# Kernel tuning notes

Hardware: AMD Instinct MI355X
Metric: run time of the kernel (lower is better)

The kernel has to match this reference:

```python
import jax, jax.numpy as jnp
import numpy as np

EPS = 0.4          # attack step size (init eps)
TOP_K_FRAC = 0.5   # fraction of tokens kept by gradient magnitude
STD_MULT = 3.0     # outlier threshold in stds
COS_EPS = 1e-8     # torch cosine_similarity norm clamp

B, S, E, V = 32, 64, 512, 50257


def setup_inputs() -> dict:
    key = jax.random.key(0)
    k1, k2, k3 = jax.random.split(key, 3)
    utterance = jax.random.randint(k1, (B, S), 0, V)
    emb_table = jax.random.normal(k2, (V, E), dtype=jnp.float32)
    data_grad = jax.random.normal(k3, (B, S, E), dtype=jnp.float32) * 0.01
    return {"utterance": utterance, "emb_table": emb_table, "data_grad": data_grad}


def fgsm_attack(inputs, data_grad):
    # inputs, data_grad: [B, S, E]
    b, s, e = data_grad.shape
    abs_grad = jnp.abs(data_grad).sum(axis=-1)                # [B, S]
    k = int(TOP_K_FRAC * s)
    _, top_idx = jax.lax.top_k(abs_grad, k)                   # [B, k], descending
    tok_mask = jnp.zeros((b, s), dtype=bool).at[jnp.arange(b)[:, None], top_idx].set(True)
    mask = jnp.broadcast_to(tok_mask[:, :, None], data_grad.shape)  # [B, S, E]
    g = jnp.where(mask, data_grad, 0.0)
    n = b * k * e                                             # number of kept gradient entries
    mean = g.sum() / n
    var = (jnp.where(mask, data_grad - mean, 0.0) ** 2).sum() / (n - 1)  # unbiased (torch.std)
    std = jnp.sqrt(var)
    lb, ub = mean - std * STD_MULT, mean + std * STD_MULT
    outside = (data_grad < lb) | (data_grad > ub)
    g2 = jnp.where(mask & outside, data_grad, 0.0)
    return inputs + EPS * jnp.sign(g2)


def reference(utterance, emb_table, data_grad):
    # embedding lookup: in_data = embeddings(utterance)
    in_data = emb_table[utterance]                            # [B, S, E]
    perturbed = fgsm_attack(in_data, data_grad)               # [B, S, E]
    # batched cosine similarity of every perturbed token vs full vocab
    p_norm = jnp.maximum(jnp.linalg.norm(perturbed, axis=-1), COS_EPS)   # [B, S]
    t_norm = jnp.maximum(jnp.linalg.norm(emb_table, axis=-1), COS_EPS)   # [V]
    sim = jnp.einsum("bse,ve->bsv", perturbed, emb_table)
    sim = sim / (p_norm[:, :, None] * t_norm[None, None, :])  # [B, S, V]
    # nearest-neighbor token ids (deterministic first-of-ties, replaces random tie sampling)
    nn_idx = jnp.argmax(sim, axis=-1)                         # [B, S]
    return nn_idx, sim
```

## Files before the change

kernel.cpp:

```cpp
#include <hip/hip_runtime.h>

#define B_      32
#define S_      64
#define E_      512
#define V_      50257
#define NPAD_   50304
#define M_      2048
#define NMASK_  524288.0
#define EPS_    0.4f

typedef _Float16 half8 __attribute__((ext_vector_type(8)));
typedef float f32x4 __attribute__((ext_vector_type(4)));

__device__ __forceinline__ float wave_sum(float s) {
#pragma unroll
    for (int d = 32; d; d >>= 1) s += __shfl_xor(s, d);
    return s;
}

__global__ void k_absgrad(const float* __restrict__ grad, float* __restrict__ absg) {
    const int row = blockIdx.x * 4 + (threadIdx.x >> 6);
    const int ln  = threadIdx.x & 63;
    const float4* g = (const float4*)(grad + (size_t)row * E_) + ln * 2;
    float4 a = g[0], b = g[1];
    float s = fabsf(a.x) + fabsf(a.y) + fabsf(a.z) + fabsf(a.w)
            + fabsf(b.x) + fabsf(b.y) + fabsf(b.z) + fabsf(b.w);
    s = wave_sum(s);
    if (ln == 0) absg[row] = s;
}

__global__ void k_topk(const float* __restrict__ absg, int* __restrict__ mask) {
    __shared__ float sh[S_];
    const int b = blockIdx.x, s = threadIdx.x;
    const float v = absg[b * S_ + s];
    sh[s] = v;
    __syncthreads();
    int rank = 0;
#pragma unroll
    for (int t = 0; t < S_; ++t) {
        float o = sh[t];
        rank += (o > v) || (o == v && t < s);
    }
    mask[b * S_ + s] = (rank < 32);
}

__global__ void k_stats1(const float* __restrict__ grad, const int* __restrict__ mask,
                         float* __restrict__ part) {
    const int tid = threadIdx.x;
    float s1 = 0.f, s2 = 0.f;
    for (int i = blockIdx.x * 256 + tid; i < M_ * E_; i += 128 * 256) {
        if (mask[i >> 9]) {
            float x = grad[i];
            s1 += x; s2 += x * x;
        }
    }
    s1 = wave_sum(s1); s2 = wave_sum(s2);
    __shared__ float r1[4], r2[4];
    if ((tid & 63) == 0) { r1[tid >> 6] = s1; r2[tid >> 6] = s2; }
    __syncthreads();
    if (tid == 0) {
        part[2 * blockIdx.x]     = r1[0] + r1[1] + r1[2] + r1[3];
        part[2 * blockIdx.x + 1] = r2[0] + r2[1] + r2[2] + r2[3];
    }
}

__global__ void k_stats2(const float* __restrict__ part, float* __restrict__ stats) {
    if (threadIdx.x == 0) {
        double s1 = 0.0, s2 = 0.0;
        for (int i = 0; i < 128; ++i) { s1 += part[2 * i]; s2 += part[2 * i + 1]; }
        const double n = NMASK_;
        double mean = s1 / n;
        double var  = (s2 - s1 * s1 / n) / (n - 1.0);
        double sd   = sqrt(var);
        stats[0] = (float)(mean - 3.0 * sd);
        stats[1] = (float)(mean + 3.0 * sd);
    }
}

__global__ void k_pert(const float* __restrict__ grad, const float* __restrict__ emb,
                       const int* __restrict__ utt, const int* __restrict__ mask,
                       const float* __restrict__ stats,
                       _Float16* __restrict__ pf16, float* __restrict__ inv_p) {
    const int row = blockIdx.x * 4 + (threadIdx.x >> 6);
    const int ln  = threadIdx.x & 63;
    const int tok = utt[row];
    const int msk = mask[row];
    const float lb = stats[0], ub = stats[1];
    const float* gp = grad + (size_t)row * E_ + ln * 8;
    const float* ep = emb + (size_t)tok * E_ + ln * 8;
    float4 g0 = *(const float4*)gp, g1 = *(const float4*)(gp + 4);
    float4 e0 = *(const float4*)ep, e1 = *(const float4*)(ep + 4);
    float gx[8] = {g0.x, g0.y, g0.z, g0.w, g1.x, g1.y, g1.z, g1.w};
    float ex[8] = {e0.x, e0.y, e0.z, e0.w, e1.x, e1.y, e1.z, e1.w};
    half8 h;
    float ss = 0.f;
#pragma unroll
    for (int i = 0; i < 8; ++i) {
        float x = gx[i];
        float val = ex[i];
        if (msk && (x < lb || x > ub)) val += (x > 0.f) ? EPS_ : -EPS_;
        ss += val * val;
        h[i] = (_Float16)val;
    }
    *(half8*)(pf16 + (size_t)row * E_ + ln * 8) = h;
    ss = wave_sum(ss);
    if (ln == 0) inv_p[row] = 1.f / fmaxf(sqrtf(ss), 1e-8f);
}

__global__ void k_emb(const float* __restrict__ emb, _Float16* __restrict__ ef16,
                      float* __restrict__ inv_t) {
    const int row = blockIdx.x * 4 + (threadIdx.x >> 6);
    const int ln  = threadIdx.x & 63;
    half8 h;
    float ss = 0.f;
    if (row < V_) {
        const float* ep = emb + (size_t)row * E_ + ln * 8;
        float4 e0 = *(const float4*)ep, e1 = *(const float4*)(ep + 4);
        float ex[8] = {e0.x, e0.y, e0.z, e0.w, e1.x, e1.y, e1.z, e1.w};
#pragma unroll
        for (int i = 0; i < 8; ++i) { ss += ex[i] * ex[i]; h[i] = (_Float16)ex[i]; }
    } else {
#pragma unroll
        for (int i = 0; i < 8; ++i) h[i] = (_Float16)0.f;
    }
    *(half8*)(ef16 + (size_t)row * E_ + ln * 8) = h;
    ss = wave_sum(ss);
    if (ln == 0) inv_t[row] = (row < V_) ? 1.f / fmaxf(sqrtf(ss), 1e-8f) : 0.f;
}

__device__ __forceinline__ void glds16(const _Float16* g, void* l) {
    __builtin_amdgcn_global_load_lds(
        (const __attribute__((address_space(1))) void*)g,
        (__attribute__((address_space(3))) void*)l, 16, 0, 0);
}

__global__ __launch_bounds__(256) void k_gemm(
    const _Float16* __restrict__ A,
    const _Float16* __restrict__ Bm,
    const float* __restrict__ inv_p,
    const float* __restrict__ inv_t,
    float* __restrict__ simout,
    unsigned long long* __restrict__ keys) {
    __shared__ _Float16 As[128][32];
    __shared__ _Float16 Bs[128][32];
    const int tid = threadIdx.x;
    const int wv = tid >> 6, ln = tid & 63;
    const int m0 = blockIdx.y * 128, n0 = blockIdx.x * 128;
    const int wr = wv >> 1, wc = wv & 1;
    const int lr = ln & 15, lk = (ln >> 4) * 8;

    f32x4 acc[4][4];
#pragma unroll
    for (int i = 0; i < 4; ++i)
#pragma unroll
        for (int j = 0; j < 4; ++j) acc[i][j] = (f32x4){0.f, 0.f, 0.f, 0.f};

    const int srow = wv * 16 + (ln >> 2);
    const int scol = (ln & 3) * 8;
    const _Float16* gA = A  + (size_t)(m0 + srow) * E_ + scol;
    const _Float16* gB = Bm + (size_t)(n0 + srow) * E_ + scol;
    char* lA = (char*)&As[0][0] + wv * 1024;
    char* lB = (char*)&Bs[0][0] + wv * 1024;

    for (int k0 = 0; k0 < E_; k0 += 32) {
        glds16(gA + k0,            lA);
        glds16(gA + 64 * E_ + k0,  lA + 4096);
        glds16(gB + k0,            lB);
        glds16(gB + 64 * E_ + k0,  lB + 4096);
        __syncthreads();
        half8 af[4], bf[4];
#pragma unroll
        for (int f = 0; f < 4; ++f) {
            af[f] = *(const half8*)&As[wr * 64 + f * 16 + lr][lk];
            bf[f] = *(const half8*)&Bs[wc * 64 + f * 16 + lr][lk];
        }
#pragma unroll
        for (int i = 0; i < 4; ++i)
#pragma unroll
            for (int j = 0; j < 4; ++j)
                acc[i][j] = __builtin_amdgcn_mfma_f32_16x16x32_f16(af[i], bf[j], acc[i][j], 0, 0, 0);
        __syncthreads();
    }

    int vv[4];
    float itv[4];
#pragma unroll
    for (int fn = 0; fn < 4; ++fn) {
        vv[fn] = n0 + wc * 64 + fn * 16 + lr;
        itv[fn] = inv_t[vv[fn]];
    }
#pragma unroll
    for (int fm = 0; fm < 4; ++fm) {
#pragma unroll
        for (int j = 0; j < 4; ++j) {
            const int m = m0 + wr * 64 + fm * 16 + (ln >> 4) * 4 + j;
            const float ip = inv_p[m];
            float* orow = simout + (size_t)m * V_;
            unsigned long long best = 0ull;
#pragma unroll
            for (int fn = 0; fn < 4; ++fn) {
                const int v = vv[fn];
                if (v < V_) {
                    const float sv = acc[fm][fn][j] * ip * itv[fn];
                    orow[v] = sv;
                    unsigned u = __float_as_uint(sv);
                    u = (u & 0x80000000u) ? ~u : (u | 0x80000000u);
                    unsigned long long e = ((unsigned long long)u << 32) | (unsigned)(~v);
                    best = e > best ? e : best;
                }
            }
#pragma unroll
            for (int d = 1; d < 16; d <<= 1) {
                unsigned long long o = __shfl_xor(best, d);
                best = o > best ? o : best;
            }
            if (lr == 0) atomicMax(keys + m, best);
        }
    }
}

__global__ void k_idx(const unsigned long long* __restrict__ keys, float* __restrict__ out) {
    const int i = blockIdx.x * 256 + threadIdx.x;
    if (i < M_) {
        unsigned v = ~(unsigned)(keys[i] & 0xFFFFFFFFull);
        out[i] = (float)v;
    }
}

extern "C" void kernel_launch(void* const* d_in, const int* in_sizes, int n_in,
                              void* d_out, int out_size, void* d_ws, size_t ws_size,
                              hipStream_t stream) {
    const int*   utt  = (const int*)d_in[0];
    const float* emb  = (const float*)d_in[1];
    const float* grad = (const float*)d_in[2];

    char* ws = (char*)d_ws;
    _Float16* embF16  = (_Float16*)(ws);
    _Float16* pertF16 = (_Float16*)(ws + 51511296);
    float* inv_t = (float*)(ws + 53608448);
    float* inv_p = (float*)(ws + 53809664);
    float* absg  = (float*)(ws + 53817856);
    int*   mask  = (int*)  (ws + 53826048);
    float* part  = (float*)(ws + 53834240);
    float* stats = (float*)(ws + 53835264);
    unsigned long long* keys = (unsigned long long*)(ws + 53835520);

    float* outIdx = (float*)d_out;
    float* simout = (float*)d_out + M_;

    hipMemsetAsync(keys, 0, M_ * 8, stream);
    k_absgrad<<<M_ / 4, 256, 0, stream>>>(grad, absg);
    k_topk<<<B_, S_, 0, stream>>>(absg, mask);
    k_stats1<<<128, 256, 0, stream>>>(grad, mask, part);
    k_stats2<<<1, 64, 0, stream>>>(part, stats);
    k_pert<<<M_ / 4, 256, 0, stream>>>(grad, emb, utt, mask, stats, pertF16, inv_p);
    k_emb<<<NPAD_ / 4, 256, 0, stream>>>(emb, embF16, inv_t);
    k_gemm<<<dim3(NPAD_ / 128, M_ / 128), 256, 0, stream>>>(pertF16, embF16, inv_p, inv_t, simout, keys);
    k_idx<<<8, 256, 0, stream>>>(keys, outIdx);
}
```

Before: 963.9 us.

## Double-buffer GEMM LDS tiles, swizzle workgroups across XCDs, parallelize stats reduction

The GEMM main loop now uses two LDS buffers, so the global-to-LDS load for the next K slice is issued before the MFMAs on the current slice run. This halves the barriers per iteration and lets loads overlap with compute. The 2D grid becomes a 1D grid whose block ids are remapped, so consecutive workgroups on the same XCD share nearby M/N tiles and should get better L2 reuse. The single-thread stats reduction is also replaced by a wave-wide shuffle reduction in double precision. The cost is twice the LDS per block, which may lower occupancy.

```diff
diff --git a/kernel.cpp b/kernel.cpp
--- a/kernel.cpp
+++ b/kernel.cpp
@@ -8,6 +8,8 @@
 #define M_      2048
 #define NMASK_  524288.0
 #define EPS_    0.4f
+#define NWG_    6288
+#define CPX_    786
 
 typedef _Float16 half8 __attribute__((ext_vector_type(8)));
 typedef float f32x4 __attribute__((ext_vector_type(4)));
@@ -65,9 +67,19 @@
 }
 
 __global__ void k_stats2(const float* __restrict__ part, float* __restrict__ stats) {
-    if (threadIdx.x == 0) {
-        double s1 = 0.0, s2 = 0.0;
-        for (int i = 0; i < 128; ++i) { s1 += part[2 * i]; s2 += part[2 * i + 1]; }
+    const int ln = threadIdx.x & 63;
+    double s1 = 0.0, s2 = 0.0;
+    if (ln < 32) { s1 = part[2 * ln]; s2 = part[2 * ln + 1]; }
+    if (ln + 64 < 128) { }
+    s1 += (double)part[2 * (ln + 64)];
+    s2 += (double)part[2 * (ln + 64) + 1];
+    if (ln >= 32) { s1 += (double)part[2 * ln]; s2 += (double)part[2 * ln + 1]; }
+#pragma unroll
+    for (int d = 32; d; d >>= 1) {
+        s1 += __shfl_xor(s1, d);
+        s2 += __shfl_xor(s2, d);
+    }
+    if (ln == 0) {
         const double n = NMASK_;
         double mean = s1 / n;
         double var  = (s2 - s1 * s1 / n) / (n - 1.0);
@@ -141,11 +153,16 @@
     const float* __restrict__ inv_t,
     float* __restrict__ simout,
     unsigned long long* __restrict__ keys) {
-    __shared__ _Float16 As[128][32];
-    __shared__ _Float16 Bs[128][32];
+    __shared__ _Float16 As[2][128][32];
+    __shared__ _Float16 Bs[2][128][32];
     const int tid = threadIdx.x;
     const int wv = tid >> 6, ln = tid & 63;
-    const int m0 = blockIdx.y * 128, n0 = blockIdx.x * 128;
+
+    const int orig = blockIdx.x;
+    const int wg = (orig & 7) * CPX_ + (orig >> 3);
+    const int m0 = (wg & 15) * 128;
+    const int n0 = (wg >> 4) * 128;
+
     const int wr = wv >> 1, wc = wv & 1;
     const int lr = ln & 15, lk = (ln >> 4) * 8;
 
@@ -159,28 +176,43 @@
     const int scol = (ln & 3) * 8;
     const _Float16* gA = A  + (size_t)(m0 + srow) * E_ + scol;
     const _Float16* gB = Bm + (size_t)(n0 + srow) * E_ + scol;
-    char* lA = (char*)&As[0][0] + wv * 1024;
-    char* lB = (char*)&Bs[0][0] + wv * 1024;
-
-    for (int k0 = 0; k0 < E_; k0 += 32) {
-        glds16(gA + k0,            lA);
-        glds16(gA + 64 * E_ + k0,  lA + 4096);
-        glds16(gB + k0,            lB);
-        glds16(gB + 64 * E_ + k0,  lB + 4096);
+
+#define STAGE(buf, k0) do {                                         \
+        char* lA_ = (char*)&As[buf][0][0] + wv * 1024;              \
+        char* lB_ = (char*)&Bs[buf][0][0] + wv * 1024;              \
+        glds16(gA + (k0),            lA_);                          \
+        glds16(gA + 64 * E_ + (k0),  lA_ + 4096);                   \
+        glds16(gB + (k0),            lB_);                          \
+        glds16(gB + 64 * E_ + (k0),  lB_ + 4096);                   \
+    } while (0)
+
+#define COMPUTE(buf) do {                                           \
+        half8 af[4], bf[4];                                         \
+        _Pragma("unroll")                                           \
+        for (int f = 0; f < 4; ++f) {                               \
+            af[f] = *(const half8*)&As[buf][wr * 64 + f * 16 + lr][lk]; \
+            bf[f] = *(const half8*)&Bs[buf][wc * 64 + f * 16 + lr][lk]; \
+        }                                                           \
+        _Pragma("unroll")                                           \
+        for (int i = 0; i < 4; ++i)                                 \
+            _Pragma("unroll")                                       \
+            for (int j = 0; j < 4; ++j)                             \
+                acc[i][j] = __builtin_amdgcn_mfma_f32_16x16x32_f16(af[i], bf[j], acc[i][j], 0, 0, 0); \
+    } while (0)
+
+    STAGE(0, 0);
+    __syncthreads();
+    int cur = 0;
+#pragma unroll 2
+    for (int t = 0; t < 15; ++t) {
+        STAGE(cur ^ 1, (t + 1) * 32);
+        COMPUTE(cur);
         __syncthreads();
-        half8 af[4], bf[4];
-#pragma unroll
-        for (int f = 0; f < 4; ++f) {
-            af[f] = *(const half8*)&As[wr * 64 + f * 16 + lr][lk];
-            bf[f] = *(const half8*)&Bs[wc * 64 + f * 16 + lr][lk];
-        }
-#pragma unroll
-        for (int i = 0; i < 4; ++i)
-#pragma unroll
-            for (int j = 0; j < 4; ++j)
-                acc[i][j] = __builtin_amdgcn_mfma_f32_16x16x32_f16(af[i], bf[j], acc[i][j], 0, 0, 0);
-        __syncthreads();
-    }
+        cur ^= 1;
+    }
+    COMPUTE(cur);
+#undef STAGE
+#undef COMPUTE
 
     int vv[4];
     float itv[4];
@@ -255,6 +287,6 @@
     k_stats2<<<1, 64, 0, stream>>>(part, stats);
     k_pert<<<M_ / 4, 256, 0, stream>>>(grad, emb, utt, mask, stats, pertF16, inv_p);
     k_emb<<<NPAD_ / 4, 256, 0, stream>>>(emb, embF16, inv_t);
-    k_gemm<<<dim3(NPAD_ / 128, M_ / 128), 256, 0, stream>>>(pertF16, embF16, inv_p, inv_t, simout, keys);
+    k_gemm<<<NWG_, 256, 0, stream>>>(pertF16, embF16, inv_p, inv_t, simout, keys);
     k_idx<<<8, 256, 0, stream>>>(keys, outIdx);
 }
```

Result: faster. 783.8 us (-18.7%).
